# Kernel optimization log

Hardware: AMD Instinct MI355X
Metric: run time of the kernel (lower is better)

Reference implementation:

```python
import jax, jax.numpy as jnp
import numpy as np

B, N, D, D_OUT = 8, 2048, 256, 256
LN_EPS = 1e-5
LRELU_SLOPE = 0.01


def setup_inputs() -> dict:
    key = jax.random.key(0)
    ks = jax.random.split(key, 11)
    s_in = 1.0 / np.sqrt(D)
    s_out = 1.0 / np.sqrt(D)
    return {
        "x_local": jax.random.normal(ks[0], (B, N, D), dtype=jnp.float32),
        "Wq": jax.random.uniform(ks[1], (D, D), jnp.float32, -s_in, s_in),
        "bq": jax.random.uniform(ks[2], (D,), jnp.float32, -s_in, s_in),
        "Wk": jax.random.uniform(ks[3], (D, D), jnp.float32, -s_in, s_in),
        "bk": jax.random.uniform(ks[4], (D,), jnp.float32, -s_in, s_in),
        "Wv": jax.random.uniform(ks[5], (D, D), jnp.float32, -s_in, s_in),
        "bv": jax.random.uniform(ks[6], (D,), jnp.float32, -s_in, s_in),
        "Wo": jax.random.uniform(ks[7], (D_OUT, D), jnp.float32, -s_out, s_out),
        "bo": jax.random.uniform(ks[8], (D_OUT,), jnp.float32, -s_out, s_out),
        "ln_gamma": jnp.ones((D_OUT,), jnp.float32),
        "ln_beta": jnp.zeros((D_OUT,), jnp.float32),
    }


def reference(x_local, Wq, bq, Wk, bk, Wv, bv, Wo, bo, ln_gamma, ln_beta):
    # Linear layers (torch convention: y = x @ W.T + b)
    Q = jnp.einsum("bnd,ed->bne", x_local, Wq) + bq
    K = jnp.einsum("bnd,ed->bne", x_local, Wk) + bk
    V = jnp.einsum("bnd,ed->bne", x_local, Wv) + bv
    # Unscaled attention (source applies no 1/sqrt(d))
    scores = jnp.einsum("bnd,bmd->bnm", Q, K)          # [B, N, N]
    attn = jax.nn.softmax(scores, axis=-1)
    loc = jnp.einsum("bnm,bmd->bnd", attn, V)           # [B, N, D]
    # fc_out: Linear -> LayerNorm -> LeakyReLU
    h = jnp.einsum("bnd,ed->bne", loc, Wo) + bo          # [B, N, D_OUT]
    mu = jnp.mean(h, axis=-1, keepdims=True)
    var = jnp.mean(jnp.square(h - mu), axis=-1, keepdims=True)
    hn = (h - mu) / jnp.sqrt(var + LN_EPS) * ln_gamma + ln_beta
    return jnp.where(hn >= 0, hn, LRELU_SLOPE * hn)
```

## Files before the change

### kernel.cpp

```cpp
#include <hip/hip_runtime.h>

typedef unsigned short u16;
typedef __attribute__((ext_vector_type(8))) _Float16 f16x8;
typedef __attribute__((ext_vector_type(4))) float f32x4;

#define MFMA_F16 __builtin_amdgcn_mfma_f32_16x16x32_f16

static __device__ __forceinline__ u16 f2h(float f) {
    return __builtin_bit_cast(u16, (_Float16)f);
}
static __device__ __forceinline__ ushort4 f4_to_h4(const float4 v) {
    ushort4 r;
    r.x = f2h(v.x); r.y = f2h(v.y); r.z = f2h(v.z); r.w = f2h(v.w);
    return r;
}

__global__ __launch_bounds__(256) void prep(
    const float* __restrict__ x,
    const float* __restrict__ wq, const float* __restrict__ wk,
    const float* __restrict__ wv, const float* __restrict__ wo,
    u16* __restrict__ xh, u16* __restrict__ w4)
{
    const int tid = blockIdx.x * 256 + threadIdx.x;
    for (int i = tid; i < 1048576; i += 2048 * 256)
        ((ushort4*)xh)[i] = f4_to_h4(((const float4*)x)[i]);
    if (blockIdx.x < 64) {
        for (int i = tid; i < 65536; i += 16384) {
            const float* src = (i < 16384) ? wq : (i < 32768) ? wk
                             : (i < 49152) ? wv : wo;
            ((ushort4*)w4)[i] = f4_to_h4(((const float4*)src)[i & 16383]);
        }
    }
}

__global__ __launch_bounds__(256) void proj_qkv(
    const u16* __restrict__ xh, const u16* __restrict__ w4,
    const float* __restrict__ bq, const float* __restrict__ bk,
    const float* __restrict__ bv,
    u16* __restrict__ Qh, u16* __restrict__ Kh, u16* __restrict__ V)
{
    const int z = blockIdx.y;
    const u16* __restrict__ W     = w4 + z * 65536;
    const float* __restrict__ bias = (z == 0) ? bq : (z == 1) ? bk : bv;
    u16* __restrict__ Y            = (z == 0) ? Qh : (z == 1) ? Kh : V;

    const int m0   = blockIdx.x * 64;
    const int t    = threadIdx.x;
    const int w    = t >> 6;
    const int lane = t & 63;
    const int quad = lane >> 4;
    const int l16  = lane & 15;

    __shared__ __align__(16) u16 Xs[64 * 40];
    __shared__ __align__(16) u16 Ws[256 * 40];

    f32x4 acc[16];
#pragma unroll
    for (int i = 0; i < 16; ++i) acc[i] = f32x4{0.f, 0.f, 0.f, 0.f};

    for (int kc = 0; kc < 8; ++kc) {
        {
            const int row = t >> 2, cg = t & 3;
            *(int4*)&Xs[row * 40 + cg * 8] =
                *(const int4*)&xh[(size_t)(m0 + row) * 256 + kc * 32 + cg * 8];
        }
#pragma unroll
        for (int i = 0; i < 4; ++i) {
            const int ch = i * 256 + t;
            const int row = ch >> 2, cg = ch & 3;
            *(int4*)&Ws[row * 40 + cg * 8] =
                *(const int4*)&W[(size_t)row * 256 + kc * 32 + cg * 8];
        }
        __syncthreads();

        const f16x8 af = *(const f16x8*)&Xs[(w * 16 + l16) * 40 + quad * 8];
#pragma unroll
        for (int nt = 0; nt < 16; ++nt) {
            const f16x8 bf = *(const f16x8*)&Ws[(nt * 16 + l16) * 40 + quad * 8];
            acc[nt] = MFMA_F16(af, bf, acc[nt], 0, 0, 0);
        }
        __syncthreads();
    }

#pragma unroll
    for (int nt = 0; nt < 16; ++nt) {
        const int col = nt * 16 + l16;
        const float bb = bias[col];
#pragma unroll
        for (int r = 0; r < 4; ++r) {
            const int row = m0 + w * 16 + quad * 4 + r;
            Y[(size_t)row * 256 + col] = f2h(acc[nt][r] + bb);
        }
    }
}

__global__ __launch_bounds__(256) void transpose_v(
    const u16* __restrict__ V, u16* __restrict__ Vt)
{
    __shared__ u16 tile[32][33];
    const int b  = blockIdx.z;
    const int n0 = blockIdx.x * 32;
    const int d0 = blockIdx.y * 32;
    const int tx = threadIdx.x;
    const int ty = threadIdx.y;
#pragma unroll
    for (int i = 0; i < 4; ++i)
        tile[ty + 8 * i][tx] =
            V[(size_t)(b * 2048 + n0 + ty + 8 * i) * 256 + d0 + tx];
    __syncthreads();
#pragma unroll
    for (int i = 0; i < 4; ++i)
        Vt[(size_t)b * 524288 + (size_t)(d0 + ty + 8 * i) * 2048 + n0 + tx] =
            tile[tx][ty + 8 * i];
}

__global__ __launch_bounds__(256) void attn(
    const u16* __restrict__ Qh, const u16* __restrict__ Kg,
    const u16* __restrict__ Vt, u16* __restrict__ Op, float* __restrict__ lmp)
{
    const int nz = gridDim.z;
    const int z  = blockIdx.z;
    const int tbase = 64 / nz, trem = 64 % nz;
    const int my_tiles = tbase + (z < trem ? 1 : 0);
    const int tile0    = tbase * z + (z < trem ? z : trem);

    const int b  = blockIdx.y;
    const int q0 = blockIdx.x * 64;
    const int t    = threadIdx.x;
    const int w    = t >> 6;
    const int lane = t & 63;
    const int quad = lane >> 4;
    const int l16  = lane & 15;

    __shared__ __align__(16) u16 smem[18688];
    u16* Ks = smem;
    u16* Vs = smem + 8448;
    u16* Os = smem;

    f16x8 qf[8];
    {
        const size_t qrow = (size_t)(b * 2048 + q0 + w * 16 + l16) * 256;
#pragma unroll
        for (int kc = 0; kc < 8; ++kc)
            qf[kc] = *(const f16x8*)&Qh[qrow + kc * 32 + quad * 8];
    }

    f32x4 O[16];
#pragma unroll
    for (int i = 0; i < 16; ++i) O[i] = f32x4{0.f, 0.f, 0.f, 0.f};
    float mrow = -1e30f, lrow = 0.f;

    for (int it = 0; it < my_tiles; ++it) {
        const int kt = (tile0 + it) * 32;
#pragma unroll
        for (int i = 0; i < 4; ++i) {
            const int ch = i * 256 + t;
            const int row = ch >> 5, cg = ch & 31;
            const int prow = ((row >> 2) & 3) * 8 + (row >> 4) * 4 + (row & 3);
            *(int4*)&Ks[row * 264 + cg * 8] =
                *(const int4*)&Kg[(size_t)(b * 2048 + kt + prow) * 256 + cg * 8];
        }
#pragma unroll
        for (int i = 0; i < 4; ++i) {
            const int ch = i * 256 + t;
            const int row = ch >> 2, cg = ch & 3;
            *(int4*)&Vs[row * 40 + cg * 8] =
                *(const int4*)&Vt[(size_t)b * 524288 + (size_t)row * 2048 + kt + cg * 8];
        }
        __syncthreads();

        f32x4 S[2];
        S[0] = f32x4{0.f, 0.f, 0.f, 0.f};
        S[1] = f32x4{0.f, 0.f, 0.f, 0.f};
#pragma unroll
        for (int kc = 0; kc < 8; ++kc) {
#pragma unroll
            for (int kn = 0; kn < 2; ++kn) {
                const f16x8 kf = *(const f16x8*)&Ks[(kn * 16 + l16) * 264 + kc * 32 + quad * 8];
                S[kn] = MFMA_F16(kf, qf[kc], S[kn], 0, 0, 0);
            }
        }

        float mt = fmaxf(fmaxf(fmaxf(S[0][0], S[0][1]), fmaxf(S[0][2], S[0][3])),
                         fmaxf(fmaxf(S[1][0], S[1][1]), fmaxf(S[1][2], S[1][3])));
        mt = fmaxf(mt, __shfl_xor(mt, 16));
        mt = fmaxf(mt, __shfl_xor(mt, 32));
        const float mnew = fmaxf(mrow, mt);
        const float a = __expf(mrow - mnew);
        float p[2][4];
        float s = 0.f;
#pragma unroll
        for (int kn = 0; kn < 2; ++kn)
#pragma unroll
            for (int r = 0; r < 4; ++r) {
                p[kn][r] = __expf(S[kn][r] - mnew);
                s += p[kn][r];
            }
        s += __shfl_xor(s, 16);
        s += __shfl_xor(s, 32);
        lrow = a * lrow + s;
        mrow = mnew;

        if (__any(a < 1.f)) {
#pragma unroll
            for (int dv = 0; dv < 16; ++dv)
#pragma unroll
                for (int r = 0; r < 4; ++r) O[dv][r] *= a;
        }

        f16x8 pf;
#pragma unroll
        for (int kn = 0; kn < 2; ++kn)
#pragma unroll
            for (int r = 0; r < 4; ++r)
                pf[kn * 4 + r] = (_Float16)p[kn][r];

#pragma unroll
        for (int dvt = 0; dvt < 16; ++dvt) {
            const f16x8 vf = *(const f16x8*)&Vs[(dvt * 16 + l16) * 40 + quad * 8];
            O[dvt] = MFMA_F16(vf, pf, O[dvt], 0, 0, 0);
        }
        __syncthreads();
    }

    {
        const float rl = 1.0f / lrow;
#pragma unroll
        for (int dvt = 0; dvt < 16; ++dvt) {
            ushort4 h4;
            h4.x = f2h(O[dvt][0] * rl);
            h4.y = f2h(O[dvt][1] * rl);
            h4.z = f2h(O[dvt][2] * rl);
            h4.w = f2h(O[dvt][3] * rl);
            *(ushort4*)&Os[(w * 16 + l16) * 264 + dvt * 16 + quad * 4] = h4;
        }
        if (quad == 0) {
            const int grow = b * 2048 + q0 + w * 16 + l16;
            lmp[z * 16384 + grow]        = lrow;
            lmp[(nz + z) * 16384 + grow] = mrow;
        }
    }
    __syncthreads();

    u16* __restrict__ Oz = Op + (size_t)z * 4194304;
    {
        const int row = t >> 2;
#pragma unroll
        for (int i = 0; i < 8; ++i) {
            const int chunk = (t & 3) * 8 + i;
            *(int4*)&Oz[(size_t)(b * 2048 + q0 + row) * 256 + chunk * 8] =
                *(const int4*)&Os[row * 264 + chunk * 8];
        }
    }
}

__global__ __launch_bounds__(256) void outproj_ln(
    const u16* __restrict__ Op, const float* __restrict__ lmp,
    const u16* __restrict__ Woh, const float* __restrict__ bo,
    const float* __restrict__ gamma, const float* __restrict__ beta,
    float* __restrict__ out, int nz)
{
    const int m0   = blockIdx.x * 64;
    const int t    = threadIdx.x;
    const int w    = t >> 6;
    const int lane = t & 63;
    const int quad = lane >> 4;
    const int l16  = lane & 15;

    __shared__ __align__(16) u16 Ls[64 * 40];
    __shared__ __align__(16) u16 Ws[256 * 40];
    __shared__ _Float16 wcs[4][64];

    if (t < 64) {
        float mm = -1e30f;
        for (int zz = 0; zz < nz; ++zz)
            mm = fmaxf(mm, lmp[(nz + zz) * 16384 + m0 + t]);
        float u[4] = {0.f, 0.f, 0.f, 0.f}, s = 0.f;
        for (int zz = 0; zz < nz; ++zz) {
            u[zz] = lmp[zz * 16384 + m0 + t] * __expf(lmp[(nz + zz) * 16384 + m0 + t] - mm);
            s += u[zz];
        }
        const float inv = 1.0f / s;
#pragma unroll
        for (int zz = 0; zz < 4; ++zz)
            wcs[zz][t] = (_Float16)((zz < nz ? u[zz] : 0.f) * inv);
    }
    __syncthreads();

    f32x4 acc[16];
#pragma unroll
    for (int i = 0; i < 16; ++i) acc[i] = f32x4{0.f, 0.f, 0.f, 0.f};

    for (int kc = 0; kc < 8; ++kc) {
        {
            const int row = t >> 2, cg = t & 3;
            const size_t off = (size_t)(m0 + row) * 256 + kc * 32 + cg * 8;
            f16x8 lw;
#pragma unroll
            for (int j = 0; j < 8; ++j) lw[j] = (_Float16)0;
#pragma unroll
            for (int zz = 0; zz < 4; ++zz) {
                const int zi = (zz < nz) ? zz : 0;
                const f16x8 o = __builtin_bit_cast(f16x8,
                    *(const int4*)&Op[(size_t)zi * 4194304 + off]);
                const _Float16 wz = wcs[zz][row];
#pragma unroll
                for (int j = 0; j < 8; ++j) lw[j] += o[j] * wz;
            }
            *(int4*)&Ls[row * 40 + cg * 8] = __builtin_bit_cast(int4, lw);
        }
#pragma unroll
        for (int i = 0; i < 4; ++i) {
            const int ch = i * 256 + t;
            const int row = ch >> 2, cg = ch & 3;
            *(int4*)&Ws[row * 40 + cg * 8] =
                *(const int4*)&Woh[(size_t)row * 256 + kc * 32 + cg * 8];
        }
        __syncthreads();

        const f16x8 af = *(const f16x8*)&Ls[(w * 16 + l16) * 40 + quad * 8];
#pragma unroll
        for (int nt = 0; nt < 16; ++nt) {
            const f16x8 bf = *(const f16x8*)&Ws[(nt * 16 + l16) * 40 + quad * 8];
            acc[nt] = MFMA_F16(af, bf, acc[nt], 0, 0, 0);
        }
        __syncthreads();
    }

    float g[16], bt[16], bb[16];
#pragma unroll
    for (int nt = 0; nt < 16; ++nt) {
        const int col = nt * 16 + l16;
        bb[nt] = bo[col]; g[nt] = gamma[col]; bt[nt] = beta[col];
    }

#pragma unroll
    for (int r = 0; r < 4; ++r) {
        float h[16];
        float sh = 0.f, sh2 = 0.f;
#pragma unroll
        for (int nt = 0; nt < 16; ++nt) {
            h[nt] = acc[nt][r] + bb[nt];
            sh  += h[nt];
            sh2 += h[nt] * h[nt];
        }
        sh  += __shfl_xor(sh, 1);  sh  += __shfl_xor(sh, 2);
        sh  += __shfl_xor(sh, 4);  sh  += __shfl_xor(sh, 8);
        sh2 += __shfl_xor(sh2, 1); sh2 += __shfl_xor(sh2, 2);
        sh2 += __shfl_xor(sh2, 4); sh2 += __shfl_xor(sh2, 8);
        const float mu  = sh * (1.f / 256.f);
        const float var = fmaxf(sh2 * (1.f / 256.f) - mu * mu, 0.f);
        const float rs  = rsqrtf(var + 1e-5f);
        const size_t row = (size_t)(m0 + w * 16 + quad * 4 + r) * 256;
#pragma unroll
        for (int nt = 0; nt < 16; ++nt) {
            const float hn = (h[nt] - mu) * rs * g[nt] + bt[nt];
            out[row + nt * 16 + l16] = (hn >= 0.f) ? hn : 0.01f * hn;
        }
    }
}

extern "C" void kernel_launch(void* const* d_in, const int* in_sizes, int n_in,
                              void* d_out, int out_size, void* d_ws, size_t ws_size,
                              hipStream_t stream)
{
    const float* x  = (const float*)d_in[0];
    const float* Wq = (const float*)d_in[1];
    const float* bq = (const float*)d_in[2];
    const float* Wk = (const float*)d_in[3];
    const float* bk = (const float*)d_in[4];
    const float* Wv = (const float*)d_in[5];
    const float* bv = (const float*)d_in[6];
    const float* Wo = (const float*)d_in[7];
    const float* bo = (const float*)d_in[8];
    const float* gm = (const float*)d_in[9];
    const float* bt = (const float*)d_in[10];
    float* out = (float*)d_out;

    const size_t BASE_U16 = 262144u + 5u * 4194304u;
    const size_t need4 = (BASE_U16 + 2u * 4194304u) * 2 + 4u * 2u * 16384u * 4u;
    const size_t need3 = (BASE_U16 + 1u * 4194304u) * 2 + 3u * 2u * 16384u * 4u;
    int nz = (ws_size >= need4) ? 4 : (ws_size >= need3) ? 3 : 2;

    u16* W4 = (u16*)d_ws;
    u16* Qh = W4 + 262144;
    u16* Kh = Qh + 4194304;
    u16* Vt = Kh + 4194304;
    u16* V  = Vt + 4194304;
    u16* xh = V  + 4194304;
    u16* Op = V;
    float* lmp = (float*)(xh + 4194304 + (size_t)(nz > 2 ? nz - 2 : 0) * 4194304);
    u16* Woh = W4 + 196608;

    prep       <<<2048,            256,        0, stream>>>(x, Wq, Wk, Wv, Wo, xh, W4);
    proj_qkv   <<<dim3(256, 3),    256,        0, stream>>>(xh, W4, bq, bk, bv, Qh, Kh, V);
    transpose_v<<<dim3(64, 8, 8),  dim3(32,8), 0, stream>>>(V, Vt);
    attn       <<<dim3(32, 8, nz), 256,        0, stream>>>(Qh, Kh, Vt, Op, lmp);
    outproj_ln <<<256,             256,        0, stream>>>(Op, lmp, Woh, bo, gm, bt, out, nz);
}
```

Baseline: 203.7 us.

## Fuse x conversion and V transpose into QKV projection, fix split-K to two

The projection kernel now reads fp32 x directly and converts to half while staging into shared memory, which removes the separate x-conversion pass and its workspace. The V projection writes its output already transposed, so the standalone transpose kernel is gone. The attention split factor is fixed at two, and the output kernel's merge is simplified to match, removing the workspace-size-dependent choice of three or four splits. In exchange, x is re-read and re-converted by each of the three projection groups, the transposed V store is strided, and the attention grid may have less parallelism when more workspace was available.

```diff
diff --git a/kernel.cpp b/kernel.cpp
--- a/kernel.cpp
+++ b/kernel.cpp
@@ -15,34 +15,28 @@
     return r;
 }
 
-__global__ __launch_bounds__(256) void prep(
-    const float* __restrict__ x,
+__global__ __launch_bounds__(256) void prep_w(
     const float* __restrict__ wq, const float* __restrict__ wk,
     const float* __restrict__ wv, const float* __restrict__ wo,
-    u16* __restrict__ xh, u16* __restrict__ w4)
+    u16* __restrict__ w4)
 {
     const int tid = blockIdx.x * 256 + threadIdx.x;
-    for (int i = tid; i < 1048576; i += 2048 * 256)
-        ((ushort4*)xh)[i] = f4_to_h4(((const float4*)x)[i]);
-    if (blockIdx.x < 64) {
-        for (int i = tid; i < 65536; i += 16384) {
-            const float* src = (i < 16384) ? wq : (i < 32768) ? wk
-                             : (i < 49152) ? wv : wo;
-            ((ushort4*)w4)[i] = f4_to_h4(((const float4*)src)[i & 16383]);
-        }
+    for (int i = tid; i < 65536; i += 16384) {
+        const float* src = (i < 16384) ? wq : (i < 32768) ? wk
+                         : (i < 49152) ? wv : wo;
+        ((ushort4*)w4)[i] = f4_to_h4(((const float4*)src)[i & 16383]);
     }
 }
 
 __global__ __launch_bounds__(256) void proj_qkv(
-    const u16* __restrict__ xh, const u16* __restrict__ w4,
+    const float* __restrict__ X, const u16* __restrict__ w4,
     const float* __restrict__ bq, const float* __restrict__ bk,
     const float* __restrict__ bv,
-    u16* __restrict__ Qh, u16* __restrict__ Kh, u16* __restrict__ V)
+    u16* __restrict__ Qh, u16* __restrict__ Kh, u16* __restrict__ Vt)
 {
     const int z = blockIdx.y;
     const u16* __restrict__ W     = w4 + z * 65536;
     const float* __restrict__ bias = (z == 0) ? bq : (z == 1) ? bk : bv;
-    u16* __restrict__ Y            = (z == 0) ? Qh : (z == 1) ? Kh : V;
 
     const int m0   = blockIdx.x * 64;
     const int t    = threadIdx.x;
@@ -59,10 +53,12 @@
     for (int i = 0; i < 16; ++i) acc[i] = f32x4{0.f, 0.f, 0.f, 0.f};
 
     for (int kc = 0; kc < 8; ++kc) {
-        {
-            const int row = t >> 2, cg = t & 3;
-            *(int4*)&Xs[row * 40 + cg * 8] =
-                *(const int4*)&xh[(size_t)(m0 + row) * 256 + kc * 32 + cg * 8];
+#pragma unroll
+        for (int i = 0; i < 2; ++i) {
+            const int ch = i * 256 + t;
+            const int row = ch >> 3, cg = ch & 7;
+            const float4 v = *(const float4*)&X[(size_t)(m0 + row) * 256 + kc * 32 + cg * 4];
+            *(ushort4*)&Xs[row * 40 + cg * 4] = f4_to_h4(v);
         }
 #pragma unroll
         for (int i = 0; i < 4; ++i) {
@@ -82,36 +78,34 @@
         __syncthreads();
     }
 
-#pragma unroll
-    for (int nt = 0; nt < 16; ++nt) {
-        const int col = nt * 16 + l16;
-        const float bb = bias[col];
-#pragma unroll
-        for (int r = 0; r < 4; ++r) {
-            const int row = m0 + w * 16 + quad * 4 + r;
-            Y[(size_t)row * 256 + col] = f2h(acc[nt][r] + bb);
-        }
-    }
-}
-
-__global__ __launch_bounds__(256) void transpose_v(
-    const u16* __restrict__ V, u16* __restrict__ Vt)
-{
-    __shared__ u16 tile[32][33];
-    const int b  = blockIdx.z;
-    const int n0 = blockIdx.x * 32;
-    const int d0 = blockIdx.y * 32;
-    const int tx = threadIdx.x;
-    const int ty = threadIdx.y;
-#pragma unroll
-    for (int i = 0; i < 4; ++i)
-        tile[ty + 8 * i][tx] =
-            V[(size_t)(b * 2048 + n0 + ty + 8 * i) * 256 + d0 + tx];
-    __syncthreads();
-#pragma unroll
-    for (int i = 0; i < 4; ++i)
-        Vt[(size_t)b * 524288 + (size_t)(d0 + ty + 8 * i) * 2048 + n0 + tx] =
-            tile[tx][ty + 8 * i];
+    if (z < 2) {
+        u16* __restrict__ Y = (z == 0) ? Qh : Kh;
+#pragma unroll
+        for (int nt = 0; nt < 16; ++nt) {
+            const int col = nt * 16 + l16;
+            const float bb = bias[col];
+#pragma unroll
+            for (int r = 0; r < 4; ++r) {
+                const int row = m0 + w * 16 + quad * 4 + r;
+                Y[(size_t)row * 256 + col] = f2h(acc[nt][r] + bb);
+            }
+        }
+    } else {
+        const int b  = m0 >> 11;
+        const int n0 = m0 & 2047;
+#pragma unroll
+        for (int nt = 0; nt < 16; ++nt) {
+            const int col = nt * 16 + l16;
+            const float bb = bias[col];
+            ushort4 h4;
+            h4.x = f2h(acc[nt][0] + bb);
+            h4.y = f2h(acc[nt][1] + bb);
+            h4.z = f2h(acc[nt][2] + bb);
+            h4.w = f2h(acc[nt][3] + bb);
+            *(ushort4*)&Vt[(size_t)b * 524288 + (size_t)col * 2048
+                           + n0 + w * 16 + quad * 4] = h4;
+        }
+    }
 }
 
 __global__ __launch_bounds__(256) void attn(
@@ -258,7 +252,7 @@
     const u16* __restrict__ Op, const float* __restrict__ lmp,
     const u16* __restrict__ Woh, const float* __restrict__ bo,
     const float* __restrict__ gamma, const float* __restrict__ beta,
-    float* __restrict__ out, int nz)
+    float* __restrict__ out)
 {
     const int m0   = blockIdx.x * 64;
     const int t    = threadIdx.x;
@@ -269,21 +263,17 @@
 
     __shared__ __align__(16) u16 Ls[64 * 40];
     __shared__ __align__(16) u16 Ws[256 * 40];
-    __shared__ _Float16 wcs[4][64];
+    __shared__ _Float16 w0s[64], w1s[64];
 
     if (t < 64) {
-        float mm = -1e30f;
-        for (int zz = 0; zz < nz; ++zz)
-            mm = fmaxf(mm, lmp[(nz + zz) * 16384 + m0 + t]);
-        float u[4] = {0.f, 0.f, 0.f, 0.f}, s = 0.f;
-        for (int zz = 0; zz < nz; ++zz) {
-            u[zz] = lmp[zz * 16384 + m0 + t] * __expf(lmp[(nz + zz) * 16384 + m0 + t] - mm);
-            s += u[zz];
-        }
-        const float inv = 1.0f / s;
-#pragma unroll
-        for (int zz = 0; zz < 4; ++zz)
-            wcs[zz][t] = (_Float16)((zz < nz ? u[zz] : 0.f) * inv);
+        const float l0 = lmp[m0 + t],          l1 = lmp[16384 + m0 + t];
+        const float mm0 = lmp[32768 + m0 + t], mm1 = lmp[49152 + m0 + t];
+        const float mm = fmaxf(mm0, mm1);
+        const float u0 = l0 * __expf(mm0 - mm);
+        const float u1 = l1 * __expf(mm1 - mm);
+        const float inv = 1.0f / (u0 + u1);
+        w0s[t] = (_Float16)(u0 * inv);
+        w1s[t] = (_Float16)(u1 * inv);
     }
     __syncthreads();
 
@@ -295,18 +285,12 @@
         {
             const int row = t >> 2, cg = t & 3;
             const size_t off = (size_t)(m0 + row) * 256 + kc * 32 + cg * 8;
+            const f16x8 o0 = __builtin_bit_cast(f16x8, *(const int4*)&Op[off]);
+            const f16x8 o1 = __builtin_bit_cast(f16x8, *(const int4*)&Op[4194304 + off]);
+            const _Float16 w0 = w0s[row], w1 = w1s[row];
             f16x8 lw;
 #pragma unroll
-            for (int j = 0; j < 8; ++j) lw[j] = (_Float16)0;
-#pragma unroll
-            for (int zz = 0; zz < 4; ++zz) {
-                const int zi = (zz < nz) ? zz : 0;
-                const f16x8 o = __builtin_bit_cast(f16x8,
-                    *(const int4*)&Op[(size_t)zi * 4194304 + off]);
-                const _Float16 wz = wcs[zz][row];
-#pragma unroll
-                for (int j = 0; j < 8; ++j) lw[j] += o[j] * wz;
-            }
+            for (int j = 0; j < 8; ++j) lw[j] = o0[j] * w0 + o1[j] * w1;
             *(int4*)&Ls[row * 40 + cg * 8] = __builtin_bit_cast(int4, lw);
         }
 #pragma unroll
@@ -377,24 +361,16 @@
     const float* bt = (const float*)d_in[10];
     float* out = (float*)d_out;
 
-    const size_t BASE_U16 = 262144u + 5u * 4194304u;
-    const size_t need4 = (BASE_U16 + 2u * 4194304u) * 2 + 4u * 2u * 16384u * 4u;
-    const size_t need3 = (BASE_U16 + 1u * 4194304u) * 2 + 3u * 2u * 16384u * 4u;
-    int nz = (ws_size >= need4) ? 4 : (ws_size >= need3) ? 3 : 2;
-
     u16* W4 = (u16*)d_ws;
     u16* Qh = W4 + 262144;
     u16* Kh = Qh + 4194304;
     u16* Vt = Kh + 4194304;
-    u16* V  = Vt + 4194304;
-    u16* xh = V  + 4194304;
-    u16* Op = V;
-    float* lmp = (float*)(xh + 4194304 + (size_t)(nz > 2 ? nz - 2 : 0) * 4194304);
+    u16* Op = Vt + 4194304;
+    float* lmp = (float*)(Op + 2 * 4194304);
     u16* Woh = W4 + 196608;
 
-    prep       <<<2048,            256,        0, stream>>>(x, Wq, Wk, Wv, Wo, xh, W4);
-    proj_qkv   <<<dim3(256, 3),    256,        0, stream>>>(xh, W4, bq, bk, bv, Qh, Kh, V);
-    transpose_v<<<dim3(64, 8, 8),  dim3(32,8), 0, stream>>>(V, Vt);
-    attn       <<<dim3(32, 8, nz), 256,        0, stream>>>(Qh, Kh, Vt, Op, lmp);
-    outproj_ln <<<256,             256,        0, stream>>>(Op, lmp, Woh, bo, gm, bt, out, nz);
-}
+    prep_w     <<<64,             256, 0, stream>>>(Wq, Wk, Wv, Wo, W4);
+    proj_qkv   <<<dim3(256, 3),   256, 0, stream>>>(x, W4, bq, bk, bv, Qh, Kh, Vt);
+    attn       <<<dim3(32, 8, 2), 256, 0, stream>>>(Qh, Kh, Vt, Op, lmp);
+    outproj_ln <<<256,            256, 0, stream>>>(Op, lmp, Woh, bo, gm, bt, out);
+}
```

After: 203.3 us. About the same (-0.2%).
